# Optimization experiments

Hardware: AMD Instinct MI355X
Metric: run time of the kernel (lower is better)

The kernel has to match this reference:

```python
import jax, jax.numpy as jnp
import numpy as np

B, D, C, OUT = 16384, 784, 2048, 10

def setup_inputs() -> dict:
    key = jax.random.key(0)
    k1, k2, k3 = jax.random.split(key, 3)
    x = jax.random.normal(k1, (B, D), dtype=jnp.float32)
    centres = jax.random.normal(k2, (C, D), dtype=jnp.float32)
    log_sigmas = jnp.zeros((C,), dtype=jnp.float32)
    W = jax.random.normal(k3, (OUT, C), dtype=jnp.float32) * (1.0 / np.sqrt(C))
    b = jnp.zeros((OUT,), dtype=jnp.float32)
    return {"x": x, "centres": centres, "log_sigmas": log_sigmas, "W": W, "b": b}

def reference(x, centres, log_sigmas, W, b):
    # (B, C, D) broadcast tensor the torch code materializes; same math).
    x2 = jnp.sum(x * x, axis=-1, keepdims=True)          # (B, 1)
    c2 = jnp.sum(centres * centres, axis=-1)             # (C,)
    d2 = jnp.maximum(x2 + c2[None, :] - 2.0 * (x @ centres.T), 0.0)  # (B, C)
    distances = jnp.sqrt(d2) / jnp.exp(log_sigmas)[None, :]          # (B, C)
    phi = jnp.exp(-(distances * distances))              # gaussian basis
    return phi @ W.T + b                                  # (B, OUT)
```

## Files before the change

### kernel.cpp

```cpp
#include <hip/hip_runtime.h>


#define B_ROWS 16384
#define D_DIM  784
#define C_DIM  2048
#define NOUT   10
#define KPAD   832
#define BK     64

typedef __attribute__((ext_vector_type(8))) __bf16 bf16x8;
typedef __attribute__((ext_vector_type(4))) float  f32x4;
typedef __attribute__((ext_vector_type(4))) unsigned short ushort4v;

__device__ __forceinline__ unsigned short f2bf(float f) {
  union { float f; unsigned int u; } v; v.f = f;
  unsigned int u = v.u;
  return (unsigned short)((u + 0x7fffu + ((u >> 16) & 1u)) >> 16);
}

__device__ __forceinline__ void async16(const unsigned short* g, unsigned short* l) {
  __builtin_amdgcn_global_load_lds((const __attribute__((address_space(1))) void*)g,
                                   (__attribute__((address_space(3))) void*)l,
                                   16, 0, 0);
}

__global__ __launch_bounds__(256) void prep_rows(const float* __restrict__ src,
                                                 unsigned short* __restrict__ dst,
                                                 float* __restrict__ sq) {
  const int row  = blockIdx.x * 4 + (threadIdx.x >> 6);
  const int lane = threadIdx.x & 63;
  const float* s = src + (size_t)row * D_DIM;
  unsigned short* d = dst + (size_t)row * KPAD;
  float acc = 0.f;
#pragma unroll
  for (int c = 0; c < 4; ++c) {
    const int ch = lane + c * 64;
    if (ch < 196) {
      const float4 v = ((const float4*)s)[ch];
      ushort4v o; o.x = f2bf(v.x); o.y = f2bf(v.y); o.z = f2bf(v.z); o.w = f2bf(v.w);
      *(ushort4v*)(d + ch * 4) = o;
      acc += v.x * v.x + v.y * v.y + v.z * v.z + v.w * v.w;
    } else if (ch < 208) {
      ushort4v z = {0, 0, 0, 0};
      *(ushort4v*)(d + ch * 4) = z;
    }
  }
#pragma unroll
  for (int off = 32; off > 0; off >>= 1) acc += __shfl_down(acc, off);
  if (lane == 0) sq[row] = acc;
}

__global__ __launch_bounds__(256) void prep_misc(const float* __restrict__ ls,
                                                 const float* __restrict__ W,
                                                 const float* __restrict__ bias,
                                                 float* __restrict__ scale,
                                                 unsigned short* __restrict__ wb,
                                                 float* __restrict__ out) {
  const int i = blockIdx.x * 256 + threadIdx.x;
  if (i < B_ROWS * NOUT) out[i] = bias[i % NOUT];
  const int j = i - B_ROWS * NOUT;
  if (j >= 0 && j < 16 * C_DIM)
    wb[j] = ((j >> 11) < NOUT) ? f2bf(W[(j >> 11) * C_DIM + (j & 2047)]) : (unsigned short)0;
  const int k = j - 16 * C_DIM;
  if (k >= 0 && k < C_DIM) scale[k] = __expf(-2.f * ls[k]);
}

__global__ __launch_bounds__(256, 4) void rbf_main(
    const unsigned short* __restrict__ xb, const unsigned short* __restrict__ cb,
    const unsigned short* __restrict__ wb,
    const float* __restrict__ x2, const float* __restrict__ c2,
    const float* __restrict__ scale, float* __restrict__ out) {
  __shared__ char smem[34816];
  unsigned short* As = (unsigned short*)smem;
  unsigned short* Bs = (unsigned short*)(smem + 16384);
  unsigned short* Ph = (unsigned short*)smem;
  __shared__ float x2s[128], c2s[128], scs[128];

  const int tid  = threadIdx.x;
  const int w    = tid >> 6;
  const int lane = tid & 63;
  const int q    = lane >> 4;
  const int l16  = lane & 15;
  const int brow = blockIdx.x * 128;
  const int bcol = blockIdx.y * 128;

  if (tid < 128) x2s[tid] = x2[brow + tid];
  else { c2s[tid - 128] = c2[bcol + tid - 128]; scs[tid - 128] = scale[bcol + tid - 128]; }

  const int srow = tid >> 3;
  const int skc  = (tid & 7) ^ (srow & 7);
  const unsigned short* gA = xb + (size_t)(brow + srow) * KPAD + skc * 8;
  const unsigned short* gB = cb + (size_t)(bcol + srow) * KPAD + skc * 8;
  unsigned short* lA = &As[w * 512];
  unsigned short* lB = &Bs[w * 512];

  const int wr = (w >> 1) * 64;
  const int wc = (w & 1) * 64;
  const int swz = l16 & 7;

  f32x4 acc[4][4] = {};

  for (int k0 = 0; k0 < KPAD; k0 += BK) {
#pragma unroll
    for (int r = 0; r < 4; ++r) {
      async16(gA + (size_t)r * 32 * KPAD + k0, lA + r * 2048);
      async16(gB + (size_t)r * 32 * KPAD + k0, lB + r * 2048);
    }
    __syncthreads();
#pragma unroll
    for (int ks = 0; ks < 2; ++ks) {
      bf16x8 af[4], bfr[4];
#pragma unroll
      for (int i = 0; i < 4; ++i)
        af[i] = *(const bf16x8*)&As[(wr + i * 16 + l16) * 64 + (((ks * 4 + q) ^ swz) << 3)];
#pragma unroll
      for (int j = 0; j < 4; ++j)
        bfr[j] = *(const bf16x8*)&Bs[(wc + j * 16 + l16) * 64 + (((ks * 4 + q) ^ swz) << 3)];
#pragma unroll
      for (int i = 0; i < 4; ++i)
#pragma unroll
        for (int j = 0; j < 4; ++j)
          acc[i][j] = __builtin_amdgcn_mfma_f32_16x16x32_bf16(af[i], bfr[j], acc[i][j], 0, 0, 0);
    }
    __syncthreads();
  }

#pragma unroll
  for (int i = 0; i < 4; ++i) {
#pragma unroll
    for (int j = 0; j < 4; ++j) {
      const int cl = wc + j * 16 + l16;
      const float c2v = c2s[cl];
      const float sc = scs[cl];
#pragma unroll
      for (int r = 0; r < 4; ++r) {
        const int rl = wr + i * 16 + q * 4 + r;
        float d2 = x2s[rl] + c2v - 2.f * acc[i][j][r];
        d2 = fmaxf(d2, 0.f);
        const float phi = __expf(-d2 * sc);
        Ph[rl * 136 + cl] = f2bf(phi);
      }
    }
  }
  __syncthreads();

  f32x4 oacc[2] = {};
#pragma unroll
  for (int kk = 0; kk < 4; ++kk) {
    const bf16x8 bw = *(const bf16x8*)&wb[(size_t)l16 * C_DIM + bcol + kk * 32 + q * 8];
#pragma unroll
    for (int mi = 0; mi < 2; ++mi) {
      const bf16x8 ap = *(const bf16x8*)&Ph[(w * 32 + mi * 16 + l16) * 136 + kk * 32 + q * 8];
      oacc[mi] = __builtin_amdgcn_mfma_f32_16x16x32_bf16(ap, bw, oacc[mi], 0, 0, 0);
    }
  }
  if (l16 < NOUT) {
#pragma unroll
    for (int mi = 0; mi < 2; ++mi)
#pragma unroll
      for (int r = 0; r < 4; ++r) {
        const int grow = brow + w * 32 + mi * 16 + q * 4 + r;
        atomicAdd(&out[grow * NOUT + l16], oacc[mi][r]);
      }
  }
}

extern "C" void kernel_launch(void* const* d_in, const int* in_sizes, int n_in,
                              void* d_out, int out_size, void* d_ws, size_t ws_size,
                              hipStream_t stream) {
  const float* x    = (const float*)d_in[0];
  const float* cen  = (const float*)d_in[1];
  const float* ls   = (const float*)d_in[2];
  const float* W    = (const float*)d_in[3];
  const float* bias = (const float*)d_in[4];
  float* out = (float*)d_out;

  unsigned char* ws = (unsigned char*)d_ws;
  unsigned short* xb  = (unsigned short*)(ws);
  unsigned short* cbf = (unsigned short*)(ws + 27262976);
  unsigned short* wb  = (unsigned short*)(ws + 30670848);
  float* x2 = (float*)(ws + 30736384);
  float* c2 = (float*)(ws + 30801920);
  float* sc = (float*)(ws + 30810112);

  prep_rows<<<B_ROWS / 4, 256, 0, stream>>>(x, xb, x2);
  prep_rows<<<C_DIM / 4, 256, 0, stream>>>(cen, cbf, c2);
  prep_misc<<<(B_ROWS * NOUT + 16 * C_DIM + C_DIM + 255) / 256, 256, 0, stream>>>(
      ls, W, bias, sc, wb, out);
  rbf_main<<<dim3(B_ROWS / 128, C_DIM / 128), 256, 0, stream>>>(xb, cbf, wb, x2, c2, sc, out);
}
```

Measured before the change: 163.9 us.

## Prepack centres into MFMA fragment layout and load B operand directly from global

Adds a prep kernel that converts the centres to bf16 and stores them in a per-fragment layout, so each lane of the main GEMM loads its B operand straight from global memory. This removes the B tile's LDS staging and reduces LDS traffic in the main loop. The epilogue now folds log2(e) into the scale and uses exp2, plus a fused fma for the distance. The risk is that B loads now come from global or L2 on the critical path with no async overlap, and the centres are read twice during prep.

```diff
diff --git a/kernel.cpp b/kernel.cpp
--- a/kernel.cpp
+++ b/kernel.cpp
@@ -6,7 +6,9 @@
 #define C_DIM  2048
 #define NOUT   10
 #define KPAD   832
-#define BK     64
+#define NKC    26
+#define NCG    128
+#define LOG2E  1.4426950408889634f
 
 typedef __attribute__((ext_vector_type(8))) __bf16 bf16x8;
 typedef __attribute__((ext_vector_type(4))) float  f32x4;
@@ -18,7 +20,7 @@
   return (unsigned short)((u + 0x7fffu + ((u >> 16) & 1u)) >> 16);
 }
 
-__device__ __forceinline__ void async16(const unsigned short* g, unsigned short* l) {
+__device__ __forceinline__ void async16(const __bf16* g, __bf16* l) {
   __builtin_amdgcn_global_load_lds((const __attribute__((address_space(1))) void*)g,
                                    (__attribute__((address_space(3))) void*)l,
                                    16, 0, 0);
@@ -43,6 +45,45 @@
     } else if (ch < 208) {
       ushort4v z = {0, 0, 0, 0};
       *(ushort4v*)(d + ch * 4) = z;
+    }
+  }
+#pragma unroll
+  for (int off = 32; off > 0; off >>= 1) acc += __shfl_down(acc, off);
+  if (lane == 0) sq[row] = acc;
+}
+
+__global__ __launch_bounds__(256) void prep_cpack(const float* __restrict__ cen,
+                                                  unsigned short* __restrict__ dst) {
+  const int tile = blockIdx.x * 4 + (threadIdx.x >> 6);
+  const int lane = threadIdx.x & 63;
+  const int kc = tile >> 7;
+  const int cg = tile & 127;
+  const int c  = cg * 16 + (lane & 15);
+  const int k  = kc * 32 + (lane >> 4) * 8;
+  ushort4v o0 = {0, 0, 0, 0}, o1 = {0, 0, 0, 0};
+  if (k + 8 <= D_DIM) {
+    const float4 v0 = *(const float4*)(cen + (size_t)c * D_DIM + k);
+    const float4 v1 = *(const float4*)(cen + (size_t)c * D_DIM + k + 4);
+    o0.x = f2bf(v0.x); o0.y = f2bf(v0.y); o0.z = f2bf(v0.z); o0.w = f2bf(v0.w);
+    o1.x = f2bf(v1.x); o1.y = f2bf(v1.y); o1.z = f2bf(v1.z); o1.w = f2bf(v1.w);
+  }
+  unsigned short* p = dst + ((size_t)tile * 64 + lane) * 8;
+  *(ushort4v*)p = o0;
+  *(ushort4v*)(p + 4) = o1;
+}
+
+__global__ __launch_bounds__(256) void prep_csq(const float* __restrict__ cen,
+                                                float* __restrict__ sq) {
+  const int row  = blockIdx.x * 4 + (threadIdx.x >> 6);
+  const int lane = threadIdx.x & 63;
+  const float* s = cen + (size_t)row * D_DIM;
+  float acc = 0.f;
+#pragma unroll
+  for (int c = 0; c < 4; ++c) {
+    const int ch = lane + c * 64;
+    if (ch < 196) {
+      const float4 v = ((const float4*)s)[ch];
+      acc += v.x * v.x + v.y * v.y + v.z * v.z + v.w * v.w;
     }
   }
 #pragma unroll
@@ -62,18 +103,17 @@
   if (j >= 0 && j < 16 * C_DIM)
     wb[j] = ((j >> 11) < NOUT) ? f2bf(W[(j >> 11) * C_DIM + (j & 2047)]) : (unsigned short)0;
   const int k = j - 16 * C_DIM;
-  if (k >= 0 && k < C_DIM) scale[k] = __expf(-2.f * ls[k]);
+  if (k >= 0 && k < C_DIM) scale[k] = __expf(-2.f * ls[k]) * LOG2E;
 }
 
 __global__ __launch_bounds__(256, 4) void rbf_main(
-    const unsigned short* __restrict__ xb, const unsigned short* __restrict__ cb,
-    const unsigned short* __restrict__ wb,
+    const __bf16* __restrict__ xb, const bf16x8* __restrict__ cbp,
+    const __bf16* __restrict__ wb,
     const float* __restrict__ x2, const float* __restrict__ c2,
     const float* __restrict__ scale, float* __restrict__ out) {
   __shared__ char smem[34816];
-  unsigned short* As = (unsigned short*)smem;
-  unsigned short* Bs = (unsigned short*)(smem + 16384);
-  unsigned short* Ph = (unsigned short*)smem;
+  __bf16* As = (__bf16*)smem;
+  __bf16* Ph = (__bf16*)smem;
   __shared__ float x2s[128], c2s[128], scs[128];
 
   const int tid  = threadIdx.x;
@@ -89,34 +129,34 @@
 
   const int srow = tid >> 3;
   const int skc  = (tid & 7) ^ (srow & 7);
-  const unsigned short* gA = xb + (size_t)(brow + srow) * KPAD + skc * 8;
-  const unsigned short* gB = cb + (size_t)(bcol + srow) * KPAD + skc * 8;
-  unsigned short* lA = &As[w * 512];
-  unsigned short* lB = &Bs[w * 512];
+  const __bf16* gA = xb + (size_t)(brow + srow) * KPAD + skc * 8;
+  __bf16* lA = As + w * 512;
 
   const int wr = (w >> 1) * 64;
   const int wc = (w & 1) * 64;
+  const int cgb = (bcol >> 4) + (w & 1) * 4;
   const int swz = l16 & 7;
 
   f32x4 acc[4][4] = {};
 
-  for (int k0 = 0; k0 < KPAD; k0 += BK) {
-#pragma unroll
-    for (int r = 0; r < 4; ++r) {
+#pragma unroll 1
+  for (int it = 0; it < NKC / 2; ++it) {
+    const int k0 = it * 64;
+#pragma unroll
+    for (int r = 0; r < 4; ++r)
       async16(gA + (size_t)r * 32 * KPAD + k0, lA + r * 2048);
-      async16(gB + (size_t)r * 32 * KPAD + k0, lB + r * 2048);
-    }
     __syncthreads();
 #pragma unroll
     for (int ks = 0; ks < 2; ++ks) {
+      const int kc = it * 2 + ks;
       bf16x8 af[4], bfr[4];
+#pragma unroll
+      for (int j = 0; j < 4; ++j)
+        bfr[j] = cbp[((size_t)kc * NCG + cgb + j) * 64 + lane];
 #pragma unroll
       for (int i = 0; i < 4; ++i)
         af[i] = *(const bf16x8*)&As[(wr + i * 16 + l16) * 64 + (((ks * 4 + q) ^ swz) << 3)];
 #pragma unroll
-      for (int j = 0; j < 4; ++j)
-        bfr[j] = *(const bf16x8*)&Bs[(wc + j * 16 + l16) * 64 + (((ks * 4 + q) ^ swz) << 3)];
-#pragma unroll
       for (int i = 0; i < 4; ++i)
 #pragma unroll
         for (int j = 0; j < 4; ++j)
@@ -127,6 +167,9 @@
 
 #pragma unroll
   for (int i = 0; i < 4; ++i) {
+    float xv[4];
+#pragma unroll
+    for (int r = 0; r < 4; ++r) xv[r] = x2s[wr + i * 16 + q * 4 + r];
 #pragma unroll
     for (int j = 0; j < 4; ++j) {
       const int cl = wc + j * 16 + l16;
@@ -135,10 +178,8 @@
 #pragma unroll
       for (int r = 0; r < 4; ++r) {
         const int rl = wr + i * 16 + q * 4 + r;
-        float d2 = x2s[rl] + c2v - 2.f * acc[i][j][r];
-        d2 = fmaxf(d2, 0.f);
-        const float phi = __expf(-d2 * sc);
-        Ph[rl * 136 + cl] = f2bf(phi);
+        const float d2 = fmaxf(fmaf(-2.f, acc[i][j][r], xv[r] + c2v), 0.f);
+        Ph[rl * 136 + cl] = (__bf16)__builtin_exp2f(-d2 * sc);
       }
     }
   }
@@ -177,15 +218,17 @@
 
   unsigned char* ws = (unsigned char*)d_ws;
   unsigned short* xb  = (unsigned short*)(ws);
-  unsigned short* cbf = (unsigned short*)(ws + 27262976);
+  unsigned short* cbp = (unsigned short*)(ws + 27262976);
   unsigned short* wb  = (unsigned short*)(ws + 30670848);
   float* x2 = (float*)(ws + 30736384);
   float* c2 = (float*)(ws + 30801920);
   float* sc = (float*)(ws + 30810112);
 
   prep_rows<<<B_ROWS / 4, 256, 0, stream>>>(x, xb, x2);
-  prep_rows<<<C_DIM / 4, 256, 0, stream>>>(cen, cbf, c2);
+  prep_cpack<<<(NKC * NCG) / 4, 256, 0, stream>>>(cen, cbp);
+  prep_csq<<<C_DIM / 4, 256, 0, stream>>>(cen, c2);
   prep_misc<<<(B_ROWS * NOUT + 16 * C_DIM + C_DIM + 255) / 256, 256, 0, stream>>>(
       ls, W, bias, sc, wb, out);
-  rbf_main<<<dim3(B_ROWS / 128, C_DIM / 128), 256, 0, stream>>>(xb, cbf, wb, x2, c2, sc, out);
-}
+  rbf_main<<<dim3(B_ROWS / 128, C_DIM / 128), 256, 0, stream>>>(
+      (const __bf16*)xb, (const bf16x8*)cbp, (const __bf16*)wb, x2, c2, sc, out);
+}
```

Result: slower. 170.7 us (+4.1%).

## Pre-pack operands into MFMA fragment layout and load directly to registers

Applied to the files above, without the earlier changes.

The prep kernels now write x and centres in a fragment-tiled bf16 layout, so each lane's MFMA operand is one contiguous 16-byte load. The main GEMM drops the LDS staging and per-step barriers and instead reads fragments straight from global memory into registers, with one-step register double buffering. Tiles change to 64 rows by 256 centres: all four waves share the A rows and each wave owns its own centre columns. The exponent becomes exp2 with log2e folded into the scale. This removes LDS traffic and synchronisation, at the cost of every wave re-reading A from global/L2 and lower occupancy (launch bounds 3).

```diff
diff --git a/kernel.cpp b/kernel.cpp
--- a/kernel.cpp
+++ b/kernel.cpp
@@ -5,49 +5,55 @@
 #define D_DIM  784
 #define C_DIM  2048
 #define NOUT   10
-#define KPAD   832
-#define BK     64
+#define NKC    26
+#define NCG    128
+#define NRG    1024
+#define LOG2E  1.4426950408889634f
 
 typedef __attribute__((ext_vector_type(8))) __bf16 bf16x8;
 typedef __attribute__((ext_vector_type(4))) float  f32x4;
-typedef __attribute__((ext_vector_type(4))) unsigned short ushort4v;
 
 __device__ __forceinline__ unsigned short f2bf(float f) {
   union { float f; unsigned int u; } v; v.f = f;
   unsigned int u = v.u;
   return (unsigned short)((u + 0x7fffu + ((u >> 16) & 1u)) >> 16);
 }
-
-__device__ __forceinline__ void async16(const unsigned short* g, unsigned short* l) {
-  __builtin_amdgcn_global_load_lds((const __attribute__((address_space(1))) void*)g,
-                                   (__attribute__((address_space(3))) void*)l,
-                                   16, 0, 0);
+__device__ __forceinline__ bf16x8 cvt8(float4 a, float4 b) {
+  union { bf16x8 v; unsigned short s[8]; } o;
+  o.s[0] = f2bf(a.x); o.s[1] = f2bf(a.y); o.s[2] = f2bf(a.z); o.s[3] = f2bf(a.w);
+  o.s[4] = f2bf(b.x); o.s[5] = f2bf(b.y); o.s[6] = f2bf(b.z); o.s[7] = f2bf(b.w);
+  return o.v;
 }
 
-__global__ __launch_bounds__(256) void prep_rows(const float* __restrict__ src,
-                                                 unsigned short* __restrict__ dst,
+template <int ROWS, int A_ORDER>
+__global__ __launch_bounds__(256) void prep_pack(const float* __restrict__ src,
+                                                 bf16x8* __restrict__ dst,
                                                  float* __restrict__ sq) {
-  const int row  = blockIdx.x * 4 + (threadIdx.x >> 6);
+  const int g    = blockIdx.x * 4 + (threadIdx.x >> 6);
   const int lane = threadIdx.x & 63;
+  const int q    = lane >> 4;
+  const int l16  = lane & 15;
+  const int row  = g * 16 + l16;
   const float* s = src + (size_t)row * D_DIM;
-  unsigned short* d = dst + (size_t)row * KPAD;
   float acc = 0.f;
-#pragma unroll
-  for (int c = 0; c < 4; ++c) {
-    const int ch = lane + c * 64;
-    if (ch < 196) {
-      const float4 v = ((const float4*)s)[ch];
-      ushort4v o; o.x = f2bf(v.x); o.y = f2bf(v.y); o.z = f2bf(v.z); o.w = f2bf(v.w);
-      *(ushort4v*)(d + ch * 4) = o;
-      acc += v.x * v.x + v.y * v.y + v.z * v.z + v.w * v.w;
-    } else if (ch < 208) {
-      ushort4v z = {0, 0, 0, 0};
-      *(ushort4v*)(d + ch * 4) = z;
+#pragma unroll 2
+  for (int kc = 0; kc < NKC; ++kc) {
+    const int k = kc * 32 + q * 8;
+    bf16x8 o = {};
+    if (k + 8 <= D_DIM) {
+      const float4 v0 = *(const float4*)(s + k);
+      const float4 v1 = *(const float4*)(s + k + 4);
+      o = cvt8(v0, v1);
+      acc += v0.x * v0.x + v0.y * v0.y + v0.z * v0.z + v0.w * v0.w +
+             v1.x * v1.x + v1.y * v1.y + v1.z * v1.z + v1.w * v1.w;
     }
+    const size_t tile = A_ORDER ? ((size_t)g * NKC + kc)
+                                : ((size_t)kc * (ROWS / 16) + g);
+    dst[tile * 64 + lane] = o;
   }
-#pragma unroll
-  for (int off = 32; off > 0; off >>= 1) acc += __shfl_down(acc, off);
-  if (lane == 0) sq[row] = acc;
+  acc += __shfl_down(acc, 32);
+  acc += __shfl_down(acc, 16);
+  if (lane < 16 && row < ROWS) sq[row] = acc;
 }
 
 __global__ __launch_bounds__(256) void prep_misc(const float* __restrict__ ls,
@@ -62,106 +68,91 @@
   if (j >= 0 && j < 16 * C_DIM)
     wb[j] = ((j >> 11) < NOUT) ? f2bf(W[(j >> 11) * C_DIM + (j & 2047)]) : (unsigned short)0;
   const int k = j - 16 * C_DIM;
-  if (k >= 0 && k < C_DIM) scale[k] = __expf(-2.f * ls[k]);
+  if (k >= 0 && k < C_DIM) scale[k] = __expf(-2.f * ls[k]) * LOG2E;
 }
 
-__global__ __launch_bounds__(256, 4) void rbf_main(
-    const unsigned short* __restrict__ xb, const unsigned short* __restrict__ cb,
-    const unsigned short* __restrict__ wb,
+__global__ __launch_bounds__(256, 3) void rbf_main(
+    const bf16x8* __restrict__ apk, const bf16x8* __restrict__ cbp,
+    const __bf16* __restrict__ wb,
     const float* __restrict__ x2, const float* __restrict__ c2,
     const float* __restrict__ scale, float* __restrict__ out) {
-  __shared__ char smem[34816];
-  unsigned short* As = (unsigned short*)smem;
-  unsigned short* Bs = (unsigned short*)(smem + 16384);
-  unsigned short* Ph = (unsigned short*)smem;
-  __shared__ float x2s[128], c2s[128], scs[128];
+  __shared__ __bf16 Ph[64 * 264];
+  __shared__ float x2s[64];
 
   const int tid  = threadIdx.x;
   const int w    = tid >> 6;
   const int lane = tid & 63;
   const int q    = lane >> 4;
   const int l16  = lane & 15;
-  const int brow = blockIdx.x * 128;
-  const int bcol = blockIdx.y * 128;
+  const int bc   = blockIdx.x;
+  const int br   = blockIdx.y;
+  const int brow = br * 64;
+  const int bcol = bc * 256;
 
-  if (tid < 128) x2s[tid] = x2[brow + tid];
-  else { c2s[tid - 128] = c2[bcol + tid - 128]; scs[tid - 128] = scale[bcol + tid - 128]; }
+  if (tid < 64) x2s[tid] = x2[brow + tid];
+  __syncthreads();
 
-  const int srow = tid >> 3;
-  const int skc  = (tid & 7) ^ (srow & 7);
-  const unsigned short* gA = xb + (size_t)(brow + srow) * KPAD + skc * 8;
-  const unsigned short* gB = cb + (size_t)(bcol + srow) * KPAD + skc * 8;
-  unsigned short* lA = &As[w * 512];
-  unsigned short* lB = &Bs[w * 512];
-
-  const int wr = (w >> 1) * 64;
-  const int wc = (w & 1) * 64;
-  const int swz = l16 & 7;
+  const bf16x8* apA = apk + ((size_t)br * 4 * NKC) * 64 + lane;
+  const bf16x8* cbw = cbp + ((size_t)(bc * 16 + w * 4)) * 64 + lane;
 
   f32x4 acc[4][4] = {};
+  bf16x8 afc[4], bfc[4], afn[4], bfn[4];
+#pragma unroll
+  for (int i = 0; i < 4; ++i) afc[i] = apA[(size_t)i * NKC * 64];
+#pragma unroll
+  for (int j = 0; j < 4; ++j) bfc[j] = cbw[(size_t)j * 64];
 
-  for (int k0 = 0; k0 < KPAD; k0 += BK) {
+#pragma unroll 2
+  for (int kc = 0; kc < NKC; ++kc) {
+    const int kn = (kc + 1 < NKC) ? kc + 1 : NKC - 1;
 #pragma unroll
-    for (int r = 0; r < 4; ++r) {
-      async16(gA + (size_t)r * 32 * KPAD + k0, lA + r * 2048);
-      async16(gB + (size_t)r * 32 * KPAD + k0, lB + r * 2048);
-    }
-    __syncthreads();
+    for (int i = 0; i < 4; ++i) afn[i] = apA[((size_t)i * NKC + kn) * 64];
 #pragma unroll
-    for (int ks = 0; ks < 2; ++ks) {
-      bf16x8 af[4], bfr[4];
+    for (int j = 0; j < 4; ++j) bfn[j] = cbw[((size_t)kn * NCG + j) * 64];
 #pragma unroll
-      for (int i = 0; i < 4; ++i)
-        af[i] = *(const bf16x8*)&As[(wr + i * 16 + l16) * 64 + (((ks * 4 + q) ^ swz) << 3)];
+    for (int i = 0; i < 4; ++i)
 #pragma unroll
       for (int j = 0; j < 4; ++j)
-        bfr[j] = *(const bf16x8*)&Bs[(wc + j * 16 + l16) * 64 + (((ks * 4 + q) ^ swz) << 3)];
+        acc[i][j] = __builtin_amdgcn_mfma_f32_16x16x32_bf16(afc[i], bfc[j], acc[i][j], 0, 0, 0);
 #pragma unroll
-      for (int i = 0; i < 4; ++i)
+    for (int i = 0; i < 4; ++i) afc[i] = afn[i];
 #pragma unroll
-        for (int j = 0; j < 4; ++j)
-          acc[i][j] = __builtin_amdgcn_mfma_f32_16x16x32_bf16(af[i], bfr[j], acc[i][j], 0, 0, 0);
-    }
-    __syncthreads();
+    for (int j = 0; j < 4; ++j) bfc[j] = bfn[j];
   }
 
 #pragma unroll
   for (int i = 0; i < 4; ++i) {
+    float xv[4];
+#pragma unroll
+    for (int r = 0; r < 4; ++r) xv[r] = x2s[i * 16 + q * 4 + r];
 #pragma unroll
     for (int j = 0; j < 4; ++j) {
-      const int cl = wc + j * 16 + l16;
-      const float c2v = c2s[cl];
-      const float sc = scs[cl];
+      const int cl = w * 64 + j * 16 + l16;
+      const float c2v = c2[bcol + cl];
+      const float sc = scale[bcol + cl];
 #pragma unroll
       for (int r = 0; r < 4; ++r) {
-        const int rl = wr + i * 16 + q * 4 + r;
-        float d2 = x2s[rl] + c2v - 2.f * acc[i][j][r];
-        d2 = fmaxf(d2, 0.f);
-        const float phi = __expf(-d2 * sc);
-        Ph[rl * 136 + cl] = f2bf(phi);
+        const int rl = i * 16 + q * 4 + r;
+        const float d2 = fmaxf(fmaf(-2.f, acc[i][j][r], xv[r] + c2v), 0.f);
+        Ph[rl * 264 + cl] = (__bf16)__builtin_exp2f(-d2 * sc);
       }
     }
   }
   __syncthreads();
 
-  f32x4 oacc[2] = {};
+  f32x4 oacc = {};
 #pragma unroll
-  for (int kk = 0; kk < 4; ++kk) {
+  for (int kk = 0; kk < 8; ++kk) {
     const bf16x8 bw = *(const bf16x8*)&wb[(size_t)l16 * C_DIM + bcol + kk * 32 + q * 8];
-#pragma unroll
-    for (int mi = 0; mi < 2; ++mi) {
-      const bf16x8 ap = *(const bf16x8*)&Ph[(w * 32 + mi * 16 + l16) * 136 + kk * 32 + q * 8];
-      oacc[mi] = __builtin_amdgcn_mfma_f32_16x16x32_bf16(ap, bw, oacc[mi], 0, 0, 0);
-    }
+    const bf16x8 ap = *(const bf16x8*)&Ph[(w * 16 + l16) * 264 + kk * 32 + q * 8];
+    oacc = __builtin_amdgcn_mfma_f32_16x16x32_bf16(ap, bw, oacc, 0, 0, 0);
   }
   if (l16 < NOUT) {
 #pragma unroll
-    for (int mi = 0; mi < 2; ++mi)
-#pragma unroll
-      for (int r = 0; r < 4; ++r) {
-        const int grow = brow + w * 32 + mi * 16 + q * 4 + r;
-        atomicAdd(&out[grow * NOUT + l16], oacc[mi][r]);
-      }
+    for (int r = 0; r < 4; ++r) {
+      const int grow = brow + w * 16 + q * 4 + r;
+      atomicAdd(&out[grow * NOUT + l16], oacc[r]);
+    }
   }
 }
 
@@ -176,16 +167,16 @@
   float* out = (float*)d_out;
 
   unsigned char* ws = (unsigned char*)d_ws;
-  unsigned short* xb  = (unsigned short*)(ws);
-  unsigned short* cbf = (unsigned short*)(ws + 27262976);
-  unsigned short* wb  = (unsigned short*)(ws + 30670848);
+  bf16x8* apk = (bf16x8*)(ws);
+  bf16x8* cbp = (bf16x8*)(ws + 27262976);
+  unsigned short* wb = (unsigned short*)(ws + 30670848);
   float* x2 = (float*)(ws + 30736384);
   float* c2 = (float*)(ws + 30801920);
   float* sc = (float*)(ws + 30810112);
 
-  prep_rows<<<B_ROWS / 4, 256, 0, stream>>>(x, xb, x2);
-  prep_rows<<<C_DIM / 4, 256, 0, stream>>>(cen, cbf, c2);
+  prep_pack<B_ROWS, 1><<<NRG / 4, 256, 0, stream>>>(x, apk, x2);
+  prep_pack<C_DIM, 0><<<NCG / 4, 256, 0, stream>>>(cen, cbp, c2);
   prep_misc<<<(B_ROWS * NOUT + 16 * C_DIM + C_DIM + 255) / 256, 256, 0, stream>>>(
       ls, W, bias, sc, wb, out);
-  rbf_main<<<dim3(B_ROWS / 128, C_DIM / 128), 256, 0, stream>>>(xb, cbf, wb, x2, c2, sc, out);
+  rbf_main<<<dim3(8, 256), 256, 0, stream>>>(apk, cbp, (const __bf16*)wb, x2, c2, sc, out);
 }
```

Result: slower. 202.9 us (+23.8%).
